# Kernel optimization log

Hardware: AMD Instinct MI355X
Metric: run time of the kernel (lower is better)

Reference implementation:

```python
import jax, jax.numpy as jnp
import numpy as np

C = 512
NH = 8
GROUPS = 32
EPS = 1e-5


def setup_inputs() -> dict:
    key = jax.random.key(0)
    ks = jax.random.split(key, 7)
    B, T, H, W = 4, 24, 32, 32
    x = jax.random.normal(ks[0], (B, C, T, H, W), dtype=jnp.float32)
    gn_w = jnp.ones((C,), jnp.float32)
    gn_b = jnp.zeros((C,), jnp.float32)
    # 1x1 Conv1d weights stored as [out_ch, in_ch] (kernel dim of size 1 dropped)
    qkv_w = jax.random.normal(ks[1], (3 * C, C), dtype=jnp.float32) / np.sqrt(C)
    qkv_b = jax.random.normal(ks[2], (3 * C,), dtype=jnp.float32) * 0.02
    proj_w = jax.random.normal(ks[3], (C, C), dtype=jnp.float32) / np.sqrt(C)
    proj_b = jax.random.normal(ks[4], (C,), dtype=jnp.float32) * 0.02
    return {"x": x, "gn_w": gn_w, "gn_b": gn_b, "qkv_w": qkv_w,
            "qkv_b": qkv_b, "proj_w": proj_w, "proj_b": proj_b}


def reference(x, gn_w, gn_b, qkv_w, qkv_b, proj_w, proj_b):
    B, Cc, T, H, W = x.shape
    hd = Cc // NH
    # [B,C,T,H,W] -> [B*H*W, C, T]
    xf = jnp.transpose(x, (0, 3, 4, 1, 2)).reshape(B * H * W, Cc, T)
    # GroupNorm over (C/G, T) per group
    xg = xf.reshape(-1, GROUPS, Cc // GROUPS, T)
    mean = xg.mean(axis=(2, 3), keepdims=True)
    var = xg.var(axis=(2, 3), keepdims=True)
    xn = ((xg - mean) * jax.lax.rsqrt(var + EPS)).reshape(-1, Cc, T)
    xn = xn * gn_w[:, None] + gn_b[:, None]
    # 1x1 conv QKV: [n, 3C, T]
    qkv = jnp.einsum('nct,dc->ndt', xn, qkv_w) + qkv_b[:, None]
    qkv = qkv.reshape(-1, 3, NH, hd, T)
    q, k, v = qkv[:, 0], qkv[:, 1], qkv[:, 2]  # each [n, h, d, T]
    scale = 1.0 / np.sqrt(hd)
    attn = jax.nn.softmax(jnp.einsum('nhdt,nhds->nhts', q, k) * scale, axis=-1)
    out = jnp.einsum('nhts,nhds->nhtd', attn, v)        # [n, h, T, d]
    out = out.transpose(0, 2, 1, 3).reshape(-1, T, Cc)   # [n, T, C]
    out = out.transpose(0, 2, 1)                         # [n, C, T]
    out = jnp.einsum('nct,dc->ndt', out, proj_w) + proj_b[:, None]
    out = out.reshape(B, H, W, Cc, T).transpose(0, 3, 4, 1, 2)
    return x + out
```

## Files before the change

### kernel.cpp

```cpp
#include <hip/hip_runtime.h>
#include <hip/hip_bf16.h>
#include <stdint.h>

#define C_    512
#define T_    24
#define HWSZ  1024
#define NN    4096
#define JTOT  98304
#define EPSV  1e-5f

typedef short short8 __attribute__((ext_vector_type(8)));
typedef short short4v __attribute__((ext_vector_type(4)));
typedef float f32x4 __attribute__((ext_vector_type(4)));

typedef __attribute__((address_space(1))) const uint32_t glob_u32;
typedef __attribute__((address_space(3))) uint32_t lds_u32;

__device__ __forceinline__ unsigned short f2bf(float f) {
  union { float f; unsigned u; } v; v.f = f;
  unsigned r = v.u + 0x7fffu + ((v.u >> 16) & 1u);
  return (unsigned short)(r >> 16);
}
__device__ __forceinline__ float bf2f(unsigned short b) {
  union { unsigned u; float f; } v; v.u = ((unsigned)b) << 16;
  return v.f;
}
__device__ __forceinline__ float bflo(uint32_t u) {
  union { unsigned u; float f; } v; v.u = u << 16; return v.f;
}
__device__ __forceinline__ float bfhi(uint32_t u) {
  union { unsigned u; float f; } v; v.u = u & 0xffff0000u; return v.f;
}
__device__ __forceinline__ uint32_t pkbf(float a, float b) {
  return (uint32_t)f2bf(a) | ((uint32_t)f2bf(b) << 16);
}

__device__ __forceinline__ void gload_lds16(const void* g, void* l) {
  __builtin_amdgcn_global_load_lds((glob_u32*)g, (lds_u32*)l, 16, 0, 0);
}

__global__ void k_cvt(const float* __restrict__ qkvw, const float* __restrict__ projw,
                      unsigned short* __restrict__ qkvw_bf, unsigned short* __restrict__ projw_bf) {
  int i = blockIdx.x * 256 + threadIdx.x;
  if (i < 786432) qkvw_bf[i] = f2bf(qkvw[i]);
  if (i < 262144) projw_bf[i] = f2bf(projw[i]);
}

__global__ __launch_bounds__(256) void k_stats(const float* __restrict__ x,
                                               float* __restrict__ mean, float* __restrict__ rstd) {
  int bid = blockIdx.x;
  int g = bid & 31, hwt = (bid >> 5) & 15, b = bid >> 9;
  int tid = threadIdx.x, lane = tid & 63, grp = tid >> 6;
  int hw = hwt * 64 + lane;
  float s = 0.f, sq = 0.f;
  for (int ct = grp; ct < 384; ct += 4) {
    int c = g * 16 + ct / 24;
    int t = ct % 24;
    float v = x[((size_t)((b * 512 + c) * 24 + t) << 10) + hw];
    s += v; sq += v * v;
  }
  __shared__ float ls[4][64], lq[4][64];
  ls[grp][lane] = s; lq[grp][lane] = sq;
  __syncthreads();
  if (tid < 64) {
    float S = ls[0][tid] + ls[1][tid] + ls[2][tid] + ls[3][tid];
    float Q = lq[0][tid] + lq[1][tid] + lq[2][tid] + lq[3][tid];
    float m = S * (1.f / 384.f);
    float var = Q * (1.f / 384.f) - m * m;
    int n = b * HWSZ + hwt * 64 + tid;
    mean[n * 32 + g] = m;
    rstd[n * 32 + g] = rsqrtf(var + EPSV);
  }
}

__global__ __launch_bounds__(256) void k_norm(const float* __restrict__ x,
                                              const float* __restrict__ mean, const float* __restrict__ rstd,
                                              const float* __restrict__ gnw, const float* __restrict__ gnb,
                                              unsigned short* __restrict__ xn) {
  __shared__ unsigned short xs[64][260];
  const int bid = blockIdx.x;
  const int hwt = bid & 15;
  const int chalf = (bid >> 4) & 1;
  const int tb = bid >> 5;
  const int t = tb % 24, b = tb / 24;
  const int hw0 = hwt * 64;
  const int tid = threadIdx.x;
  const int w = tid >> 6, lane = tid & 63;

  const int cslot = w * 4 + (lane >> 4);
  const int hwr = (lane & 15) * 4;
#pragma unroll
  for (int k = 0; k < 8; ++k) {
    const int crel = k * 32 + cslot * 2;
    const int c = chalf * 256 + crel;
    const float4 v0 = *reinterpret_cast<const float4*>(
        &x[(((size_t)(b * 512 + c) * 24 + t) << 10) + hw0 + hwr]);
    const float4 v1 = *reinterpret_cast<const float4*>(
        &x[(((size_t)(b * 512 + c + 1) * 24 + t) << 10) + hw0 + hwr]);
    *reinterpret_cast<uint32_t*>(&xs[hwr + 0][crel]) = pkbf(v0.x, v1.x);
    *reinterpret_cast<uint32_t*>(&xs[hwr + 1][crel]) = pkbf(v0.y, v1.y);
    *reinterpret_cast<uint32_t*>(&xs[hwr + 2][crel]) = pkbf(v0.z, v1.z);
    *reinterpret_cast<uint32_t*>(&xs[hwr + 3][crel]) = pkbf(v0.w, v1.w);
  }

  const int crel8 = (lane & 31) * 8;
  const int c8 = chalf * 256 + crel8;
  const int g = c8 >> 4;
  float gw[8], gb[8];
#pragma unroll
  for (int i = 0; i < 8; ++i) { gw[i] = gnw[c8 + i]; gb[i] = gnb[c8 + i]; }
  float mm[8], rr[8];
#pragma unroll
  for (int p = 0; p < 8; ++p) {
    const int nrel = (p * 4 + w) * 2 + (lane >> 5);
    const int ng = b * HWSZ + hw0 + nrel;
    mm[p] = mean[ng * 32 + g];
    rr[p] = rstd[ng * 32 + g];
  }
  __syncthreads();

#pragma unroll
  for (int p = 0; p < 8; ++p) {
    const int nrel = (p * 4 + w) * 2 + (lane >> 5);
    const short4v lo = *reinterpret_cast<const short4v*>(&xs[nrel][crel8]);
    const short4v hi = *reinterpret_cast<const short4v*>(&xs[nrel][crel8 + 4]);
    float y[8];
#pragma unroll
    for (int i = 0; i < 4; ++i) {
      y[i]     = (bf2f((unsigned short)lo[i]) - mm[p]) * rr[p] * gw[i]     + gb[i];
      y[i + 4] = (bf2f((unsigned short)hi[i]) - mm[p]) * rr[p] * gw[i + 4] + gb[i + 4];
    }
    uint4 wv;
    wv.x = pkbf(y[0], y[1]);
    wv.y = pkbf(y[2], y[3]);
    wv.z = pkbf(y[4], y[5]);
    wv.w = pkbf(y[6], y[7]);
    const size_t j = (size_t)t * NN + b * HWSZ + hw0 + nrel;
    *reinterpret_cast<uint4*>(&xn[j * C_ + c8]) = wv;
  }
}

#define STAGE8(mat, half, tile, Gptr, row0)                                           \
  {                                                                                   \
    unsigned short* _l = &lds[(((tile) & 1) * 2 + (mat))][half][(w * 2) * 512];       \
    const unsigned short* _g = (Gptr) +                                               \
        (size_t)((row0) + (half) * 128 + (w * 2) * 8 + srow) * 512 +                  \
        (tile) * 64 + sslot * 8;                                                      \
    gload_lds16(_g, _l);                                                              \
    gload_lds16(_g + 8 * 512, _l + 512);                                              \
  }

__global__ __launch_bounds__(512, 2) void k_gemm8(
    const unsigned short* __restrict__ A,
    const unsigned short* __restrict__ B,
    const float* __restrict__ bias,
    unsigned short* __restrict__ outb) {
  __shared__ __attribute__((aligned(16))) unsigned short lds[4][2][8192];
  const int bid = blockIdx.x;
  const int cpx = gridDim.x >> 3;
  const int lid = (bid & 7) * cpx + (bid >> 3);
  const int mt = lid & 1, jt = lid >> 1;
  const int m0 = mt * 256, j0 = jt * 256;
  const int tid = threadIdx.x;
  const int w = tid >> 6, lane = tid & 63;
  const int l16 = lane & 15, lqq = lane >> 4;
  const int wm = w >> 2, wn = w & 3;
  const int srow = lane >> 3;
  const int sslot = (lane & 7) ^ srow;
  const int k0off = l16 * 64 + ((lqq ^ (l16 & 7)) * 8);
  const int k1off = l16 * 64 + (((lqq + 4) ^ (l16 & 7)) * 8);

  f32x4 acc[8][4];
#pragma unroll
  for (int i = 0; i < 8; ++i)
#pragma unroll
    for (int j = 0; j < 4; ++j) acc[i][j] = {0.f, 0.f, 0.f, 0.f};

  STAGE8(0, 0, 0, A, m0); STAGE8(0, 1, 0, A, m0);
  STAGE8(1, 0, 0, B, j0); STAGE8(1, 1, 0, B, j0);
  STAGE8(0, 0, 1, A, m0); STAGE8(0, 1, 1, A, m0);
  STAGE8(1, 0, 1, B, j0);
  asm volatile("s_waitcnt vmcnt(6)" ::: "memory");
  __builtin_amdgcn_s_barrier();

  for (int t = 0; t < 8; ++t) {
    const int buf = t & 1;
    const unsigned short* Ab = &lds[buf * 2 + 0][wm][0];
    const unsigned short* Bb = &lds[buf * 2 + 1][wn >> 1][(wn & 1) * 4096];
    short8 a[8][2], bb[4][2];
#pragma unroll
    for (int rr = 0; rr < 8; ++rr) {
      a[rr][0] = *reinterpret_cast<const short8*>(Ab + rr * 1024 + k0off);
      a[rr][1] = *reinterpret_cast<const short8*>(Ab + rr * 1024 + k1off);
    }
#pragma unroll
    for (int cc = 0; cc < 2; ++cc) {
      bb[cc][0] = *reinterpret_cast<const short8*>(Bb + cc * 1024 + k0off);
      bb[cc][1] = *reinterpret_cast<const short8*>(Bb + cc * 1024 + k1off);
    }
    if (t < 7) STAGE8(1, 1, t + 1, B, j0);
    asm volatile("" ::: "memory");
    __builtin_amdgcn_s_barrier();
    asm volatile("s_waitcnt lgkmcnt(0)" ::: "memory");
    __builtin_amdgcn_sched_barrier(0);
    __builtin_amdgcn_s_setprio(1);
#pragma unroll
    for (int rr = 0; rr < 4; ++rr)
#pragma unroll
      for (int cc = 0; cc < 2; ++cc) {
        acc[rr][cc] = __builtin_amdgcn_mfma_f32_16x16x32_bf16(a[rr][0], bb[cc][0], acc[rr][cc], 0, 0, 0);
        acc[rr][cc] = __builtin_amdgcn_mfma_f32_16x16x32_bf16(a[rr][1], bb[cc][1], acc[rr][cc], 0, 0, 0);
      }
    __builtin_amdgcn_s_setprio(0);
    asm volatile("" ::: "memory");
    __builtin_amdgcn_s_barrier();
#pragma unroll
    for (int cc = 2; cc < 4; ++cc) {
      bb[cc][0] = *reinterpret_cast<const short8*>(Bb + cc * 1024 + k0off);
      bb[cc][1] = *reinterpret_cast<const short8*>(Bb + cc * 1024 + k1off);
    }
    if (t < 6) STAGE8(0, 0, t + 2, A, m0);
    asm volatile("" ::: "memory");
    __builtin_amdgcn_s_barrier();
    asm volatile("s_waitcnt lgkmcnt(0)" ::: "memory");
    __builtin_amdgcn_sched_barrier(0);
    __builtin_amdgcn_s_setprio(1);
#pragma unroll
    for (int rr = 0; rr < 4; ++rr)
#pragma unroll
      for (int cc = 2; cc < 4; ++cc) {
        acc[rr][cc] = __builtin_amdgcn_mfma_f32_16x16x32_bf16(a[rr][0], bb[cc][0], acc[rr][cc], 0, 0, 0);
        acc[rr][cc] = __builtin_amdgcn_mfma_f32_16x16x32_bf16(a[rr][1], bb[cc][1], acc[rr][cc], 0, 0, 0);
      }
    __builtin_amdgcn_s_setprio(0);
    asm volatile("" ::: "memory");
    __builtin_amdgcn_s_barrier();
    if (t < 6) STAGE8(0, 1, t + 2, A, m0);
    asm volatile("" ::: "memory");
    __builtin_amdgcn_s_barrier();
    __builtin_amdgcn_s_setprio(1);
#pragma unroll
    for (int rr = 4; rr < 8; ++rr)
#pragma unroll
      for (int cc = 0; cc < 2; ++cc) {
        acc[rr][cc] = __builtin_amdgcn_mfma_f32_16x16x32_bf16(a[rr][0], bb[cc][0], acc[rr][cc], 0, 0, 0);
        acc[rr][cc] = __builtin_amdgcn_mfma_f32_16x16x32_bf16(a[rr][1], bb[cc][1], acc[rr][cc], 0, 0, 0);
      }
    __builtin_amdgcn_s_setprio(0);
    asm volatile("" ::: "memory");
    __builtin_amdgcn_s_barrier();
    if (t < 6) STAGE8(1, 0, t + 2, B, j0);
    asm volatile("" ::: "memory");
    __builtin_amdgcn_s_barrier();
    __builtin_amdgcn_s_setprio(1);
#pragma unroll
    for (int rr = 4; rr < 8; ++rr)
#pragma unroll
      for (int cc = 2; cc < 4; ++cc) {
        acc[rr][cc] = __builtin_amdgcn_mfma_f32_16x16x32_bf16(a[rr][0], bb[cc][0], acc[rr][cc], 0, 0, 0);
        acc[rr][cc] = __builtin_amdgcn_mfma_f32_16x16x32_bf16(a[rr][1], bb[cc][1], acc[rr][cc], 0, 0, 0);
      }
    __builtin_amdgcn_s_setprio(0);
    asm volatile("" ::: "memory");
    if (t < 6) {
      asm volatile("s_waitcnt vmcnt(6)" ::: "memory");
    } else if (t == 6) {
      asm volatile("s_waitcnt vmcnt(0)" ::: "memory");
    }
    __builtin_amdgcn_s_barrier();
  }

#pragma unroll
  for (int rr = 0; rr < 8; ++rr) {
#pragma unroll
    for (int cc = 0; cc < 4; ++cc) {
      const int row = m0 + wm * 128 + rr * 16 + lqq * 4;
      const int col = j0 + wn * 64 + cc * 16 + l16;
#pragma unroll
      for (int r = 0; r < 4; ++r) {
        float v = acc[rr][cc][r] + bias[row + r];
        outb[(size_t)(row + r) * JTOT + col] = f2bf(v);
      }
    }
  }
}

__global__ __launch_bounds__(256, 3) void k_proj(
    const unsigned short* __restrict__ A,
    const unsigned short* __restrict__ B,
    const float* __restrict__ bias,
    const float* __restrict__ xres,
    float* __restrict__ outf) {
  __shared__ __attribute__((aligned(16))) unsigned short As[2][8192];
  const int bid = blockIdx.x;
  const int cpx = 3072 >> 3;
  const int lid = (bid & 7) * cpx + (bid >> 3);
  const int mt = lid & 3, jt = lid >> 2;
  const int m0 = mt * 128, j0 = jt * 128;
  const int tid = threadIdx.x;
  const int w = tid >> 6, lane = tid & 63;
  const int l16 = lane & 15, lqq = lane >> 4;
  const int wm = w >> 1, wn = w & 1;
  const int srow8 = lane >> 3;
  const int sslot = (lane & 7) ^ srow8;
  const int k0off = l16 * 64 + ((lqq ^ (l16 & 7)) * 8);
  const int k1off = l16 * 64 + (((lqq + 4) ^ (l16 & 7)) * 8);

  f32x4 acc[4][4];
#pragma unroll
  for (int i = 0; i < 4; ++i)
#pragma unroll
    for (int j = 0; j < 4; ++j) acc[i][j] = {0.f, 0.f, 0.f, 0.f};

#define PSTAGE(buf, tile)                                                             \
  {                                                                                   \
    _Pragma("unroll")                                                                 \
    for (int m_ = 0; m_ < 4; ++m_) {                                                  \
      unsigned short* _l = &As[buf][m_ * 2048 + w * 512];                             \
      const unsigned short* _g = A +                                                  \
          (size_t)(m0 + m_ * 32 + w * 8 + srow8) * 512 + (tile) * 64 + sslot * 8;     \
      gload_lds16(_g, _l);                                                            \
    }                                                                                 \
  }

#define LOADB(dst, tt)                                                                \
  {                                                                                   \
    _Pragma("unroll")                                                                 \
    for (int cc = 0; cc < 4; ++cc) {                                                  \
      const int jj_ = j0 + wn * 64 + cc * 16 + l16;                                   \
      _Pragma("unroll")                                                               \
      for (int ks = 0; ks < 2; ++ks)                                                  \
        dst[cc][ks] = *reinterpret_cast<const short8*>(                               \
            &B[((size_t)((tt) * 8 + ks * 4 + lqq) * JTOT + jj_) * 8]);                \
    }                                                                                 \
  }

#define PSTEP(t, CUR, NXT)                                                            \
  {                                                                                   \
    if ((t) < 7) { PSTAGE(((t) + 1) & 1, (t) + 1); LOADB(NXT, (t) + 1); }             \
    const unsigned short* Ab = &As[(t) & 1][(wm * 64) * 64];                          \
    _Pragma("unroll")                                                                 \
    for (int rr = 0; rr < 4; ++rr) {                                                  \
      short8 a0 = *reinterpret_cast<const short8*>(Ab + rr * 1024 + k0off);           \
      short8 a1 = *reinterpret_cast<const short8*>(Ab + rr * 1024 + k1off);           \
      _Pragma("unroll")                                                               \
      for (int cc = 0; cc < 4; ++cc) {                                                \
        acc[rr][cc] = __builtin_amdgcn_mfma_f32_16x16x32_bf16(a0, CUR[cc][0], acc[rr][cc], 0, 0, 0); \
        acc[rr][cc] = __builtin_amdgcn_mfma_f32_16x16x32_bf16(a1, CUR[cc][1], acc[rr][cc], 0, 0, 0); \
      }                                                                               \
    }                                                                                 \
    __syncthreads();                                                                  \
  }

  short8 bbA[4][2], bbB[4][2];
  PSTAGE(0, 0);
  LOADB(bbA, 0);
  __syncthreads();

  PSTEP(0, bbA, bbB);
  PSTEP(1, bbB, bbA);
  PSTEP(2, bbA, bbB);
  PSTEP(3, bbB, bbA);
  PSTEP(4, bbA, bbB);
  PSTEP(5, bbB, bbA);
  PSTEP(6, bbA, bbB);
  PSTEP(7, bbB, bbA);

#pragma unroll
  for (int mi = 0; mi < 4; ++mi) {
#pragma unroll
    for (int ni = 0; ni < 4; ++ni) {
      const int dbase = m0 + wm * 64 + mi * 16 + lqq * 4;
      const int jj = j0 + wn * 64 + ni * 16 + l16;
      const int t_ = jj >> 12, n = jj & 4095;
      const int b_ = n >> 10, hw = n & 1023;
#pragma unroll
      for (int r = 0; r < 4; ++r) {
        size_t o = (((size_t)(b_ * 512 + dbase + r) * 24 + t_) << 10) + hw;
        outf[o] = xres[o] + acc[mi][ni][r] + bias[dbase + r];
      }
    }
  }
}

__global__ __launch_bounds__(512) void k_attn(const unsigned short* __restrict__ qkv,
                                              unsigned short* __restrict__ aoC) {
  __shared__ uint32_t kbuf[4][24][64];
  const int ntile = blockIdx.x, h = blockIdx.y;
  const int n0 = ntile * 64;
  const int lane = threadIdx.x & 63, slot = threadIdx.x >> 6;
  const int t0 = slot * 3;
  const size_t baseq = (size_t)(h * 64) * JTOT + n0 + lane;
  const size_t basek = (size_t)(512 + h * 64) * JTOT + n0 + lane;
  const size_t basev = (size_t)(1024 + h * 64) * JTOT + n0 + lane;

  float S[3][24];
#pragma unroll
  for (int a = 0; a < 3; ++a)
#pragma unroll
    for (int s = 0; s < 24; ++s) S[a][s] = 0.f;

  uint32_t kp[12], qp[12];

#pragma unroll
  for (int dp = 0; dp < 4; ++dp)
#pragma unroll
    for (int a = 0; a < 3; ++a) {
      uint32_t klo = qkv[basek + (size_t)(2 * dp) * JTOT + (t0 + a) * NN];
      uint32_t khi = qkv[basek + (size_t)(2 * dp + 1) * JTOT + (t0 + a) * NN];
      kp[dp * 3 + a] = klo | (khi << 16);
      uint32_t qlo = qkv[baseq + (size_t)(2 * dp) * JTOT + (t0 + a) * NN];
      uint32_t qhi = qkv[baseq + (size_t)(2 * dp + 1) * JTOT + (t0 + a) * NN];
      qp[dp * 3 + a] = qlo | (qhi << 16);
    }

  for (int c = 0; c < 8; ++c) {
    const int dc = c * 8;
#pragma unroll
    for (int dp = 0; dp < 4; ++dp)
#pragma unroll
      for (int a = 0; a < 3; ++a)
        kbuf[dp][t0 + a][lane] = kp[dp * 3 + a];
    float qf[3][8];
#pragma unroll
    for (int dp = 0; dp < 4; ++dp)
#pragma unroll
      for (int a = 0; a < 3; ++a) {
        qf[a][2 * dp]     = bflo(qp[dp * 3 + a]);
        qf[a][2 * dp + 1] = bfhi(qp[dp * 3 + a]);
      }
    if (c < 7) {
      const int dn = dc + 8;
#pragma unroll
      for (int dp = 0; dp < 4; ++dp)
#pragma unroll
        for (int a = 0; a < 3; ++a) {
          uint32_t klo = qkv[basek + (size_t)(dn + 2 * dp) * JTOT + (t0 + a) * NN];
          uint32_t khi = qkv[basek + (size_t)(dn + 2 * dp + 1) * JTOT + (t0 + a) * NN];
          kp[dp * 3 + a] = klo | (khi << 16);
          uint32_t qlo = qkv[baseq + (size_t)(dn + 2 * dp) * JTOT + (t0 + a) * NN];
          uint32_t qhi = qkv[baseq + (size_t)(dn + 2 * dp + 1) * JTOT + (t0 + a) * NN];
          qp[dp * 3 + a] = qlo | (qhi << 16);
        }
    }
    __syncthreads();
#pragma unroll
    for (int dp = 0; dp < 4; ++dp) {
#pragma unroll
      for (int s = 0; s < 24; ++s) {
        uint32_t kpr = kbuf[dp][s][lane];
        float k0 = bflo(kpr), k1 = bfhi(kpr);
        S[0][s] = fmaf(qf[0][2 * dp], k0, S[0][s]);
        S[0][s] = fmaf(qf[0][2 * dp + 1], k1, S[0][s]);
        S[1][s] = fmaf(qf[1][2 * dp], k0, S[1][s]);
        S[1][s] = fmaf(qf[1][2 * dp + 1], k1, S[1][s]);
        S[2][s] = fmaf(qf[2][2 * dp], k0, S[2][s]);
        S[2][s] = fmaf(qf[2][2 * dp + 1], k1, S[2][s]);
      }
    }
    __syncthreads();
  }

#pragma unroll
  for (int dp = 0; dp < 4; ++dp)
#pragma unroll
    for (int a = 0; a < 3; ++a) {
      uint32_t vlo = qkv[basev + (size_t)(2 * dp) * JTOT + (t0 + a) * NN];
      uint32_t vhi = qkv[basev + (size_t)(2 * dp + 1) * JTOT + (t0 + a) * NN];
      kp[dp * 3 + a] = vlo | (vhi << 16);
    }

#pragma unroll
  for (int a = 0; a < 3; ++a) {
    float mx = S[a][0];
#pragma unroll
    for (int s = 1; s < 24; ++s) mx = fmaxf(mx, S[a][s]);
    float sum = 0.f;
#pragma unroll
    for (int s = 0; s < 24; ++s) {
      float e = __expf((S[a][s] - mx) * 0.125f);
      S[a][s] = e; sum += e;
    }
    float inv = 1.f / sum;
#pragma unroll
    for (int s = 0; s < 24; ++s) S[a][s] *= inv;
  }

  for (int c = 0; c < 8; ++c) {
    const int dc = c * 8;
#pragma unroll
    for (int dp = 0; dp < 4; ++dp)
#pragma unroll
      for (int a = 0; a < 3; ++a)
        kbuf[dp][t0 + a][lane] = kp[dp * 3 + a];
    if (c < 7) {
      const int dn = dc + 8;
#pragma unroll
      for (int dp = 0; dp < 4; ++dp)
#pragma unroll
        for (int a = 0; a < 3; ++a) {
          uint32_t vlo = qkv[basev + (size_t)(dn + 2 * dp) * JTOT + (t0 + a) * NN];
          uint32_t vhi = qkv[basev + (size_t)(dn + 2 * dp + 1) * JTOT + (t0 + a) * NN];
          kp[dp * 3 + a] = vlo | (vhi << 16);
        }
    }
    __syncthreads();
    float o[3][8];
#pragma unroll
    for (int a = 0; a < 3; ++a)
#pragma unroll
      for (int d = 0; d < 8; ++d) o[a][d] = 0.f;
#pragma unroll
    for (int dp = 0; dp < 4; ++dp) {
#pragma unroll
      for (int s = 0; s < 24; ++s) {
        uint32_t vpr = kbuf[dp][s][lane];
        float v0 = bflo(vpr), v1 = bfhi(vpr);
        o[0][2 * dp]     = fmaf(S[0][s], v0, o[0][2 * dp]);
        o[0][2 * dp + 1] = fmaf(S[0][s], v1, o[0][2 * dp + 1]);
        o[1][2 * dp]     = fmaf(S[1][s], v0, o[1][2 * dp]);
        o[1][2 * dp + 1] = fmaf(S[1][s], v1, o[1][2 * dp + 1]);
        o[2][2 * dp]     = fmaf(S[2][s], v0, o[2][2 * dp]);
        o[2][2 * dp + 1] = fmaf(S[2][s], v1, o[2][2 * dp + 1]);
      }
    }
#pragma unroll
    for (int a = 0; a < 3; ++a) {
      uint4 wv;
      wv.x = pkbf(o[a][0], o[a][1]);
      wv.y = pkbf(o[a][2], o[a][3]);
      wv.z = pkbf(o[a][4], o[a][5]);
      wv.w = pkbf(o[a][6], o[a][7]);
      size_t unit = (size_t)(h * 8 + c) * JTOT + (size_t)(t0 + a) * NN + n0 + lane;
      *reinterpret_cast<uint4*>(&aoC[unit * 8]) = wv;
    }
    __syncthreads();
  }
}

extern "C" void kernel_launch(void* const* d_in, const int* in_sizes, int n_in,
                              void* d_out, int out_size, void* d_ws, size_t ws_size,
                              hipStream_t stream) {
  (void)in_sizes; (void)n_in; (void)out_size; (void)ws_size;
  const float* x     = (const float*)d_in[0];
  const float* gnw   = (const float*)d_in[1];
  const float* gnb   = (const float*)d_in[2];
  const float* qkvw  = (const float*)d_in[3];
  const float* qkvb  = (const float*)d_in[4];
  const float* projw = (const float*)d_in[5];
  const float* projb = (const float*)d_in[6];
  float* out = (float*)d_out;
  char* ws = (char*)d_ws;

  unsigned short* qkvw_bf = (unsigned short*)(ws);
  unsigned short* projw_bf = (unsigned short*)(ws + 1572864);
  float* mean = (float*)(ws + 2097152);
  float* rstd = (float*)(ws + 2621440);
  unsigned short* xn  = (unsigned short*)(ws + 3145728);
  unsigned short* qkv = (unsigned short*)(ws + 3145728 + 100663296);

  k_cvt<<<dim3(3072), dim3(256), 0, stream>>>(qkvw, projw, qkvw_bf, projw_bf);
  k_stats<<<dim3(2048), dim3(256), 0, stream>>>(x, mean, rstd);
  k_norm<<<dim3(3072), dim3(256), 0, stream>>>(x, mean, rstd, gnw, gnb, xn);
  for (int p = 0; p < 3; ++p)
    k_gemm8<<<dim3(768), dim3(512), 0, stream>>>(qkvw_bf + (size_t)p * 512 * 512, xn,
                                                 qkvb + p * 512, qkv + (size_t)p * 512 * JTOT);
  k_attn<<<dim3(64, 8), dim3(512), 0, stream>>>(qkv, xn);
  k_proj<<<dim3(3072), dim3(256), 0, stream>>>(projw_bf, xn, projb, x, out);
}
```

Baseline: 596.4 us.

## Merge QKV GEMM launches and stage attention Q/K/V via vectorized cooperative loads

The three per-slice QKV GEMM launches become a single 2304-block launch that covers all six 256-row M tiles, with the block-to-tile mapping changed to divide by 6. The attention kernel drops per-thread 2-byte strided global loads held in registers and instead has the whole block cooperatively load 16-byte vectors of K/Q (and later V), interleave pairs of d rows, and write them into shared memory. Q now also comes from shared memory. The aim is to cut launch overhead and uncoalesced narrow loads. The cost is losing the register prefetch overlap, since loads now sit between barriers, and using twice the shared memory.

```diff
diff --git a/kernel.cpp b/kernel.cpp
--- a/kernel.cpp
+++ b/kernel.cpp
@@ -157,9 +157,9 @@
     unsigned short* __restrict__ outb) {
   __shared__ __attribute__((aligned(16))) unsigned short lds[4][2][8192];
   const int bid = blockIdx.x;
-  const int cpx = gridDim.x >> 3;
+  const int cpx = 2304 >> 3;
   const int lid = (bid & 7) * cpx + (bid >> 3);
-  const int mt = lid & 1, jt = lid >> 1;
+  const int mt = lid % 6, jt = lid / 6;
   const int m0 = mt * 256, j0 = jt * 256;
   const int tid = threadIdx.x;
   const int w = tid >> 6, lane = tid & 63;
@@ -385,14 +385,67 @@
 
 __global__ __launch_bounds__(512) void k_attn(const unsigned short* __restrict__ qkv,
                                               unsigned short* __restrict__ aoC) {
-  __shared__ uint32_t kbuf[4][24][64];
+  __shared__ uint32_t kq[2][4][24][64];
   const int ntile = blockIdx.x, h = blockIdx.y;
   const int n0 = ntile * 64;
-  const int lane = threadIdx.x & 63, slot = threadIdx.x >> 6;
+  const int tid = threadIdx.x;
+  const int lane = tid & 63, slot = tid >> 6;
   const int t0 = slot * 3;
-  const size_t baseq = (size_t)(h * 64) * JTOT + n0 + lane;
-  const size_t basek = (size_t)(512 + h * 64) * JTOT + n0 + lane;
-  const size_t basev = (size_t)(1024 + h * 64) * JTOT + n0 + lane;
+  const size_t bq = (size_t)(h * 64) * JTOT;
+  const size_t bk = (size_t)(512 + h * 64) * JTOT;
+  const size_t bv = (size_t)(1024 + h * 64) * JTOT;
+
+#define STG_UNIT(matbase, dpv, ttv, segv, dst)                                        \
+  {                                                                                   \
+    const size_t gb = (matbase) + (size_t)(dc + 2 * (dpv)) * JTOT + (ttv) * NN +      \
+                      n0 + (segv) * 8;                                                \
+    const uint4 va = *reinterpret_cast<const uint4*>(&qkv[gb]);                       \
+    const uint4 vb = *reinterpret_cast<const uint4*>(&qkv[gb + JTOT]);                \
+    uint4 w0, w1;                                                                     \
+    w0.x = (va.x & 0xffffu) | (vb.x << 16);                                           \
+    w0.y = (va.x >> 16) | (vb.x & 0xffff0000u);                                       \
+    w0.z = (va.y & 0xffffu) | (vb.y << 16);                                           \
+    w0.w = (va.y >> 16) | (vb.y & 0xffff0000u);                                       \
+    w1.x = (va.z & 0xffffu) | (vb.z << 16);                                           \
+    w1.y = (va.z >> 16) | (vb.z & 0xffff0000u);                                       \
+    w1.z = (va.w & 0xffffu) | (vb.w << 16);                                           \
+    w1.w = (va.w >> 16) | (vb.w & 0xffff0000u);                                       \
+    uint32_t* d_ = &(dst)[dpv][ttv][(segv) * 8];                                      \
+    *reinterpret_cast<uint4*>(d_) = w0;                                               \
+    *reinterpret_cast<uint4*>(d_ + 4) = w1;                                           \
+  }
+
+#define STAGE_QK(c_)                                                                  \
+  {                                                                                   \
+    const int dc = (c_) * 8;                                                          \
+    _Pragma("unroll")                                                                 \
+    for (int p = 0; p < 3; ++p) {                                                     \
+      const int row = p * 64 + (tid >> 3);                                            \
+      const int seg = tid & 7;                                                        \
+      if (row < 96) {                                                                 \
+        const int dp = row / 24, tt = row % 24;                                       \
+        STG_UNIT(bk, dp, tt, seg, kq[0]);                                             \
+      } else {                                                                        \
+        const int r2 = row - 96;                                                      \
+        const int dp = r2 / 24, tt = r2 % 24;                                         \
+        STG_UNIT(bq, dp, tt, seg, kq[1]);                                             \
+      }                                                                               \
+    }                                                                                 \
+  }
+
+#define STAGE_V(c_)                                                                   \
+  {                                                                                   \
+    const int dc = (c_) * 8;                                                          \
+    _Pragma("unroll")                                                                 \
+    for (int p = 0; p < 2; ++p) {                                                     \
+      const int u = p * 512 + tid;                                                    \
+      if (u < 768) {                                                                  \
+        const int row = u >> 3, seg = u & 7;                                          \
+        const int dp = row / 24, tt = row % 24;                                       \
+        STG_UNIT(bv, dp, tt, seg, kq[0]);                                             \
+      }                                                                               \
+    }                                                                                 \
+  }
 
   float S[3][24];
 #pragma unroll
@@ -400,56 +453,24 @@
 #pragma unroll
     for (int s = 0; s < 24; ++s) S[a][s] = 0.f;
 
-  uint32_t kp[12], qp[12];
-
-#pragma unroll
-  for (int dp = 0; dp < 4; ++dp)
-#pragma unroll
-    for (int a = 0; a < 3; ++a) {
-      uint32_t klo = qkv[basek + (size_t)(2 * dp) * JTOT + (t0 + a) * NN];
-      uint32_t khi = qkv[basek + (size_t)(2 * dp + 1) * JTOT + (t0 + a) * NN];
-      kp[dp * 3 + a] = klo | (khi << 16);
-      uint32_t qlo = qkv[baseq + (size_t)(2 * dp) * JTOT + (t0 + a) * NN];
-      uint32_t qhi = qkv[baseq + (size_t)(2 * dp + 1) * JTOT + (t0 + a) * NN];
-      qp[dp * 3 + a] = qlo | (qhi << 16);
-    }
-
+  STAGE_QK(0);
+  __syncthreads();
   for (int c = 0; c < 8; ++c) {
-    const int dc = c * 8;
+    float qf[3][8];
 #pragma unroll
     for (int dp = 0; dp < 4; ++dp)
 #pragma unroll
-      for (int a = 0; a < 3; ++a)
-        kbuf[dp][t0 + a][lane] = kp[dp * 3 + a];
-    float qf[3][8];
-#pragma unroll
-    for (int dp = 0; dp < 4; ++dp)
-#pragma unroll
       for (int a = 0; a < 3; ++a) {
-        qf[a][2 * dp]     = bflo(qp[dp * 3 + a]);
-        qf[a][2 * dp + 1] = bfhi(qp[dp * 3 + a]);
-      }
-    if (c < 7) {
-      const int dn = dc + 8;
-#pragma unroll
-      for (int dp = 0; dp < 4; ++dp)
-#pragma unroll
-        for (int a = 0; a < 3; ++a) {
-          uint32_t klo = qkv[basek + (size_t)(dn + 2 * dp) * JTOT + (t0 + a) * NN];
-          uint32_t khi = qkv[basek + (size_t)(dn + 2 * dp + 1) * JTOT + (t0 + a) * NN];
-          kp[dp * 3 + a] = klo | (khi << 16);
-          uint32_t qlo = qkv[baseq + (size_t)(dn + 2 * dp) * JTOT + (t0 + a) * NN];
-          uint32_t qhi = qkv[baseq + (size_t)(dn + 2 * dp + 1) * JTOT + (t0 + a) * NN];
-          qp[dp * 3 + a] = qlo | (qhi << 16);
-        }
-    }
-    __syncthreads();
+        const uint32_t qpr = kq[1][dp][t0 + a][lane];
+        qf[a][2 * dp]     = bflo(qpr);
+        qf[a][2 * dp + 1] = bfhi(qpr);
+      }
 #pragma unroll
     for (int dp = 0; dp < 4; ++dp) {
 #pragma unroll
       for (int s = 0; s < 24; ++s) {
-        uint32_t kpr = kbuf[dp][s][lane];
-        float k0 = bflo(kpr), k1 = bfhi(kpr);
+        const uint32_t kpr = kq[0][dp][s][lane];
+        const float k0 = bflo(kpr), k1 = bfhi(kpr);
         S[0][s] = fmaf(qf[0][2 * dp], k0, S[0][s]);
         S[0][s] = fmaf(qf[0][2 * dp + 1], k1, S[0][s]);
         S[1][s] = fmaf(qf[1][2 * dp], k0, S[1][s]);
@@ -459,16 +480,11 @@
       }
     }
     __syncthreads();
-  }
-
-#pragma unroll
-  for (int dp = 0; dp < 4; ++dp)
-#pragma unroll
-    for (int a = 0; a < 3; ++a) {
-      uint32_t vlo = qkv[basev + (size_t)(2 * dp) * JTOT + (t0 + a) * NN];
-      uint32_t vhi = qkv[basev + (size_t)(2 * dp + 1) * JTOT + (t0 + a) * NN];
-      kp[dp * 3 + a] = vlo | (vhi << 16);
-    }
+    if (c < 7) {
+      STAGE_QK(c + 1);
+      __syncthreads();
+    }
+  }
 
 #pragma unroll
   for (int a = 0; a < 3; ++a) {
@@ -486,25 +502,9 @@
     for (int s = 0; s < 24; ++s) S[a][s] *= inv;
   }
 
+  STAGE_V(0);
+  __syncthreads();
   for (int c = 0; c < 8; ++c) {
-    const int dc = c * 8;
-#pragma unroll
-    for (int dp = 0; dp < 4; ++dp)
-#pragma unroll
-      for (int a = 0; a < 3; ++a)
-        kbuf[dp][t0 + a][lane] = kp[dp * 3 + a];
-    if (c < 7) {
-      const int dn = dc + 8;
-#pragma unroll
-      for (int dp = 0; dp < 4; ++dp)
-#pragma unroll
-        for (int a = 0; a < 3; ++a) {
-          uint32_t vlo = qkv[basev + (size_t)(dn + 2 * dp) * JTOT + (t0 + a) * NN];
-          uint32_t vhi = qkv[basev + (size_t)(dn + 2 * dp + 1) * JTOT + (t0 + a) * NN];
-          kp[dp * 3 + a] = vlo | (vhi << 16);
-        }
-    }
-    __syncthreads();
     float o[3][8];
 #pragma unroll
     for (int a = 0; a < 3; ++a)
@@ -514,8 +514,8 @@
     for (int dp = 0; dp < 4; ++dp) {
 #pragma unroll
       for (int s = 0; s < 24; ++s) {
-        uint32_t vpr = kbuf[dp][s][lane];
-        float v0 = bflo(vpr), v1 = bfhi(vpr);
+        const uint32_t vpr = kq[0][dp][s][lane];
+        const float v0 = bflo(vpr), v1 = bfhi(vpr);
         o[0][2 * dp]     = fmaf(S[0][s], v0, o[0][2 * dp]);
         o[0][2 * dp + 1] = fmaf(S[0][s], v1, o[0][2 * dp + 1]);
         o[1][2 * dp]     = fmaf(S[1][s], v0, o[1][2 * dp]);
@@ -531,10 +531,14 @@
       wv.y = pkbf(o[a][2], o[a][3]);
       wv.z = pkbf(o[a][4], o[a][5]);
       wv.w = pkbf(o[a][6], o[a][7]);
-      size_t unit = (size_t)(h * 8 + c) * JTOT + (size_t)(t0 + a) * NN + n0 + lane;
+      const size_t unit = (size_t)(h * 8 + c) * JTOT + (size_t)(t0 + a) * NN + n0 + lane;
       *reinterpret_cast<uint4*>(&aoC[unit * 8]) = wv;
     }
     __syncthreads();
+    if (c < 7) {
+      STAGE_V(c + 1);
+      __syncthreads();
+    }
   }
 }
 
@@ -562,9 +566,7 @@
   k_cvt<<<dim3(3072), dim3(256), 0, stream>>>(qkvw, projw, qkvw_bf, projw_bf);
   k_stats<<<dim3(2048), dim3(256), 0, stream>>>(x, mean, rstd);
   k_norm<<<dim3(3072), dim3(256), 0, stream>>>(x, mean, rstd, gnw, gnb, xn);
-  for (int p = 0; p < 3; ++p)
-    k_gemm8<<<dim3(768), dim3(512), 0, stream>>>(qkvw_bf + (size_t)p * 512 * 512, xn,
-                                                 qkvb + p * 512, qkv + (size_t)p * 512 * JTOT);
+  k_gemm8<<<dim3(2304), dim3(512), 0, stream>>>(qkvw_bf, xn, qkvb, qkv);
   k_attn<<<dim3(64, 8), dim3(512), 0, stream>>>(qkv, xn);
   k_proj<<<dim3(3072), dim3(256), 0, stream>>>(projw_bf, xn, projb, x, out);
 }
```

Result: faster. 576.3 us (-3.4%).
